# Kernel tuning notes

Measured on AMD Instinct MI355X. Metric: run time of the kernel, lower is better.

## Reference

```python
import jax, jax.numpy as jnp
import numpy as np

NUM_STEPS = 100  # constructor default


def setup_inputs() -> dict:
    key = jax.random.key(0)
    x = jax.random.uniform(key, (2048, 1024), dtype=jnp.float32)  # [batch, features] in [0,1]
    return {"x": x}


def reference(x) -> jnp.ndarray:
    """Latency-encoding branch of TemporalSpikeCoder.encode, vectorized.

    Torch original: spike_times = ((1 - x) * num_steps).long(); then a Python
    double loop writes spike_train[b, t, f] = 1.0 when t < num_steps.
    Here that is a single masked one-hot comparison along the time axis.
    """
    spike_times = ((1.0 - x) * NUM_STEPS).astype(jnp.int32)        # [B, F]
    t = jnp.arange(NUM_STEPS, dtype=jnp.int32)                      # [T]
    # one-hot over time; entries with spike_times == NUM_STEPS (x == 0)
    # match no t in [0, NUM_STEPS) and therefore stay zero, exactly like
    # the `if t < num_steps` guard in the original.
    spike_train = (spike_times[:, None, :] == t[None, :, None]).astype(jnp.float32)  # [B, T, F]
    return spike_train
```

## Files before the change

kernel.cpp:

```cpp
#include <hip/hip_runtime.h>
#include <hip/hip_bf16.h>


constexpr int F  = 1024;
constexpr int T  = 100;
constexpr int F4 = F / 4;

__global__ __launch_bounds__(F4) void TemporalSpikeCoder_78125455114738_kernel(
    const float* __restrict__ x, float* __restrict__ out) {
    const int b  = blockIdx.x;
    const int f4 = threadIdx.x;

    const float4 xv = reinterpret_cast<const float4*>(x)[(size_t)b * F4 + f4];
    const int st0 = (int)((1.0f - xv.x) * 100.0f);
    const int st1 = (int)((1.0f - xv.y) * 100.0f);
    const int st2 = (int)((1.0f - xv.z) * 100.0f);
    const int st3 = (int)((1.0f - xv.w) * 100.0f);

    float4* o = reinterpret_cast<float4*>(out) + (size_t)b * (T * F4) + f4;
    #pragma unroll 5
    for (int t = 0; t < T; ++t) {
        float4 v;
        v.x = (st0 == t) ? 1.0f : 0.0f;
        v.y = (st1 == t) ? 1.0f : 0.0f;
        v.z = (st2 == t) ? 1.0f : 0.0f;
        v.w = (st3 == t) ? 1.0f : 0.0f;
        o[(size_t)t * F4] = v;
    }
}

extern "C" void kernel_launch(void* const* d_in, const int* in_sizes, int n_in,
                              void* d_out, int out_size, void* d_ws, size_t ws_size,
                              hipStream_t stream) {
    const float* x = (const float*)d_in[0];
    float* out = (float*)d_out;
    const int B = in_sizes[0] / F;
    TemporalSpikeCoder_78125455114738_kernel<<<B, F4, 0, stream>>>(x, out);
}
```

Measured before the change: 812.4 us.

## Flatten output into grid-stride loop with nontemporal vector stores

Replaces the one-block-per-batch-row kernel, which looped over time steps, with a grid-stride loop over every float4 of the output. Each iteration recomputes the spike time from a reread of x and writes with nontemporal stores. The aim is to spread the large write-bound output more evenly across a fixed grid and bypass cache pollution. In exchange x is reread up to T times, which should mostly hit in cache, and each element pays an integer division.

```diff
diff --git a/kernel.cpp b/kernel.cpp
--- a/kernel.cpp
+++ b/kernel.cpp
@@ -6,26 +6,28 @@
 constexpr int T  = 100;
 constexpr int F4 = F / 4;
 
-__global__ __launch_bounds__(F4) void TemporalSpikeCoder_78125455114738_kernel(
-    const float* __restrict__ x, float* __restrict__ out) {
-    const int b  = blockIdx.x;
-    const int f4 = threadIdx.x;
+typedef float v4f __attribute__((ext_vector_type(4)));
 
-    const float4 xv = reinterpret_cast<const float4*>(x)[(size_t)b * F4 + f4];
-    const int st0 = (int)((1.0f - xv.x) * 100.0f);
-    const int st1 = (int)((1.0f - xv.y) * 100.0f);
-    const int st2 = (int)((1.0f - xv.z) * 100.0f);
-    const int st3 = (int)((1.0f - xv.w) * 100.0f);
+__global__ __launch_bounds__(256) void TemporalSpikeCoder_78125455114738_kernel(
+    const float* __restrict__ x, float* __restrict__ out, int total4) {
+    const int gsz = gridDim.x * blockDim.x;
+    const v4f* __restrict__ x4 = reinterpret_cast<const v4f*>(x);
+    v4f* __restrict__ o4 = reinterpret_cast<v4f*>(out);
 
-    float4* o = reinterpret_cast<float4*>(out) + (size_t)b * (T * F4) + f4;
-    #pragma unroll 5
-    for (int t = 0; t < T; ++t) {
-        float4 v;
-        v.x = (st0 == t) ? 1.0f : 0.0f;
-        v.y = (st1 == t) ? 1.0f : 0.0f;
-        v.z = (st2 == t) ? 1.0f : 0.0f;
-        v.w = (st3 == t) ? 1.0f : 0.0f;
-        o[(size_t)t * F4] = v;
+    for (int i = blockIdx.x * blockDim.x + threadIdx.x; i < total4; i += gsz) {
+        const unsigned f4 = (unsigned)i & (F4 - 1);
+        const unsigned bt = (unsigned)i >> 8;
+        const unsigned b  = bt / T;
+        const int      t  = (int)(bt - b * T);
+
+        const v4f xv = x4[b * F4 + f4];
+        v4f v;
+        v.x = ((int)((1.0f - xv.x) * 100.0f) == t) ? 1.0f : 0.0f;
+        v.y = ((int)((1.0f - xv.y) * 100.0f) == t) ? 1.0f : 0.0f;
+        v.z = ((int)((1.0f - xv.z) * 100.0f) == t) ? 1.0f : 0.0f;
+        v.w = ((int)((1.0f - xv.w) * 100.0f) == t) ? 1.0f : 0.0f;
+
+        __builtin_nontemporal_store(v, &o4[i]);
     }
 }
 
@@ -34,6 +36,8 @@
                               hipStream_t stream) {
     const float* x = (const float*)d_in[0];
     float* out = (float*)d_out;
-    const int B = in_sizes[0] / F;
-    TemporalSpikeCoder_78125455114738_kernel<<<B, F4, 0, stream>>>(x, out);
+    const int total4 = out_size / 4;
+    const int block = 256;
+    const int grid = 2048;
+    TemporalSpikeCoder_78125455114738_kernel<<<grid, block, 0, stream>>>(x, out, total4);
 }
```

Result: slower. 856.0 us (+5.4%).
